# Kernel tuning notes

Measured on AMD Instinct MI355X. Metric: run time of the kernel, lower is better.

## Reference

```python
import jax, jax.numpy as jnp
import numpy as np

NUM_HEADS = 8
HEAD_SIZE = 64  # hidden_dim // num_heads = 512 // 8
SCALE = 1.0 / np.sqrt(HEAD_SIZE).astype(np.float32)
CAUSAL = True


def setup_inputs() -> dict:
    key = jax.random.key(0)
    k1, k2, k3 = jax.random.split(key, 3)
    b, s, d = 4, 2048, 512
    x = jax.random.normal(k1, (b, s, d), dtype=jnp.float32)
    w_qkv = jax.random.normal(k2, (d, 3 * d), dtype=jnp.float32) * 0.02
    b_qkv = jnp.zeros((3 * d,), dtype=jnp.float32)
    w_out = jax.random.normal(k3, (d, d), dtype=jnp.float32) * 0.02
    b_out = jnp.zeros((d,), dtype=jnp.float32)
    return {"x": x, "w_qkv": w_qkv, "b_qkv": b_qkv, "w_out": w_out, "b_out": b_out}


def reference(x, w_qkv, b_qkv, w_out, b_out):
    b, s, d = x.shape
    h, hd = NUM_HEADS, HEAD_SIZE
    qkv = x @ w_qkv + b_qkv                      # (b, s, 3d)
    q, k, v = jnp.split(qkv, 3, axis=-1)
    # (b, s, d) -> (b, h, s, hd)
    q = q.reshape(b, s, h, hd).transpose(0, 2, 1, 3)
    k = k.reshape(b, s, h, hd).transpose(0, 2, 1, 3)
    v = v.reshape(b, s, h, hd).transpose(0, 2, 1, 3)
    scores = jnp.einsum('bhqd,bhkd->bhqk', q, k) * SCALE  # (b, h, s, s)
    if CAUSAL:
        causal_mask = jnp.triu(jnp.ones((s, s), dtype=bool), k=1)
        scores = jnp.where(causal_mask, -jnp.inf, scores)
    attn = jax.nn.softmax(scores, axis=-1)
    out = jnp.einsum('bhqk,bhkd->bhqd', attn, v)          # (b, h, s, hd)
    out = out.transpose(0, 2, 1, 3).reshape(b, s, d)
    return out @ w_out + b_out
```

## Files before the change

kernel.cpp:

```cpp
#include <hip/hip_runtime.h>
#include <hip/hip_bf16.h>

#define BATCH 4
#define SEQ   2048
#define DM    512
#define NH    8
#define HD    64
#define PART  (BATCH*NH*SEQ*HD)
#define QSCALE 0.18033688f

typedef unsigned short u16;
typedef unsigned int   u32;
typedef __bf16 bf16x8 __attribute__((ext_vector_type(8)));
typedef float  f32x4  __attribute__((ext_vector_type(4)));
typedef float  f32x16 __attribute__((ext_vector_type(16)));
typedef unsigned int u32x2 __attribute__((ext_vector_type(2)));

__device__ __forceinline__ u16 f2bf(float f) {
    union { float f; u32 u; } v; v.f = f;
    u32 r = v.u + 0x7fffu + ((v.u >> 16) & 1u);
    return (u16)(r >> 16);
}

__device__ __forceinline__ void glds16(const u16* g, u16* lds) {
    __builtin_amdgcn_global_load_lds(
        (const __attribute__((address_space(1))) void*)g,
        (__attribute__((address_space(3))) void*)lds, 16, 0, 0);
}

__device__ __forceinline__ void pl32swap(u32 &a, u32 &b) {
    u32x2 r = __builtin_amdgcn_permlane32_swap(a, b, false, false);
    a = r[0]; b = r[1];
}

__global__ __launch_bounds__(256) void prep_k(
    const float* __restrict__ x, u16* __restrict__ xb,
    const float* __restrict__ w_qkv, u16* __restrict__ t_qkv,
    const float* __restrict__ w_out, u16* __restrict__ t_out)
{
    __shared__ u16 Ts[64][72];
    const int z = blockIdx.z, bx = blockIdx.x, t = threadIdx.x;

    if (z == 0) {
        const int n8 = PART / 8;
        for (int i = bx * 256 + t; i < n8; i += 512 * 256) {
            float4 a = *(const float4*)(x + (size_t)i * 8);
            float4 b = *(const float4*)(x + (size_t)i * 8 + 4);
            union { uint4 v; u16 s[8]; } o;
            o.s[0] = f2bf(a.x); o.s[1] = f2bf(a.y);
            o.s[2] = f2bf(a.z); o.s[3] = f2bf(a.w);
            o.s[4] = f2bf(b.x); o.s[5] = f2bf(b.y);
            o.s[6] = f2bf(b.z); o.s[7] = f2bf(b.w);
            *(uint4*)(xb + (size_t)i * 8) = o.v;
        }
        return;
    }
    const int N = (z == 1) ? 3 * DM : DM;
    const int ntiles = N / 64;
    if (bx >= ntiles * 8) return;
    const float* W = (z == 1) ? w_qkv : w_out;
    u16* Wt = (z == 1) ? t_qkv : t_out;
    const int n0 = (bx % ntiles) * 64, k0 = (bx / ntiles) * 64;

    #pragma unroll
    for (int l = 0; l < 4; ++l) {
        int idx = l * 1024 + t * 4;
        int r = idx >> 6, c = idx & 63;
        float4 v = *(const float4*)(W + (size_t)(k0 + r) * N + n0 + c);
        Ts[c + 0][r] = f2bf(v.x);
        Ts[c + 1][r] = f2bf(v.y);
        Ts[c + 2][r] = f2bf(v.z);
        Ts[c + 3][r] = f2bf(v.w);
    }
    __syncthreads();
    #pragma unroll
    for (int l = 0; l < 2; ++l) {
        int idx = l * 256 + t;
        int row = idx >> 3, ch = idx & 7;
        *(uint4*)(Wt + (size_t)(n0 + row) * DM + k0 + ch * 8) =
            *(const uint4*)(&Ts[row][ch * 8]);
    }
}

template<int MODE>
__global__ __launch_bounds__(256) void gemm_k(
    const u16* __restrict__ A, const u16* __restrict__ Bt,
    const float* __restrict__ bias, void* __restrict__ outv,
    int M, int N, int K)
{
    constexpr int BM = (MODE == 1) ? 64 : 128;
    constexpr int NI = (MODE == 1) ? 2 : 4;

    __shared__ __align__(16) u16 As[2][BM * 32];
    __shared__ __align__(16) u16 Bs[2][128 * 32];

    const int tid  = threadIdx.x;
    const int bm0  = blockIdx.x * BM;
    const int bn0  = blockIdx.y * 128;
    const int wave = tid >> 6, lane = tid & 63;
    const int l16  = lane & 15, quad = lane >> 4;
    const int wr   = (MODE == 1) ? 0 : (wave & 1) * 64;
    const int wc   = (MODE == 1) ? wave * 32 : (wave >> 1) * 64;

    const int srow = (lane >> 2);
    const int scol = (lane & 3) * 8;
    const int arow = (MODE == 1) ? (wave * 16) : (wave * 32);
    const u16* Ag = A + (size_t)(bm0 + arow + srow) * K + scol;
    const u16* Bg = Bt + (size_t)(bn0 + wave * 32 + srow) * K + scol;
    const int wofsA = arow * 32;
    const int wofsB = (wave * 32) * 32;

    f32x4 acc[4][NI];
    #pragma unroll
    for (int i = 0; i < 4; ++i)
        #pragma unroll
        for (int j = 0; j < NI; ++j)
            acc[i][j] = (f32x4){0.f, 0.f, 0.f, 0.f};

    glds16(Ag, &As[0][wofsA]);
    if (MODE == 0) glds16(Ag + (size_t)16 * K, &As[0][wofsA + 16 * 32]);
    glds16(Bg,                  &Bs[0][wofsB]);
    glds16(Bg + (size_t)16 * K, &Bs[0][wofsB + 16 * 32]);
    __syncthreads();

    const int NIT = K >> 5;
    for (int it = 0; it < NIT; ++it) {
        const int cur = it & 1;
        if (it + 1 < NIT) {
            const int nx = cur ^ 1;
            const int k0 = (it + 1) << 5;
            glds16(Ag + k0, &As[nx][wofsA]);
            if (MODE == 0) glds16(Ag + k0 + (size_t)16 * K, &As[nx][wofsA + 16 * 32]);
            glds16(Bg + k0,                  &Bs[nx][wofsB]);
            glds16(Bg + k0 + (size_t)16 * K, &Bs[nx][wofsB + 16 * 32]);
        }

        bf16x8 af[4], bfr[NI];
        #pragma unroll
        for (int mi = 0; mi < 4; ++mi)
            af[mi] = *(const bf16x8*)(&As[cur][(wr + mi * 16 + l16) * 32 + quad * 8]);
        #pragma unroll
        for (int ni = 0; ni < NI; ++ni)
            bfr[ni] = *(const bf16x8*)(&Bs[cur][(wc + ni * 16 + l16) * 32 + quad * 8]);
        #pragma unroll
        for (int mi = 0; mi < 4; ++mi)
            #pragma unroll
            for (int ni = 0; ni < NI; ++ni)
                acc[mi][ni] = __builtin_amdgcn_mfma_f32_16x16x32_bf16(
                    af[mi], bfr[ni], acc[mi][ni], 0, 0, 0);
        __syncthreads();
    }

    #pragma unroll
    for (int mi = 0; mi < 4; ++mi) {
        #pragma unroll
        for (int ni = 0; ni < NI; ++ni) {
            int col = bn0 + wc + ni * 16 + l16;
            float bv = bias[col];
            int row0 = bm0 + wr + mi * 16 + quad * 4;
            float v[4];
            #pragma unroll
            for (int reg = 0; reg < 4; ++reg) v[reg] = acc[mi][ni][reg] + bv;

            if (MODE == 1) {
                #pragma unroll
                for (int reg = 0; reg < 4; ++reg)
                    ((float*)outv)[(size_t)(row0 + reg) * N + col] = v[reg];
            } else {
                u16* ws = (u16*)outv;
                int part = col >> 9, wi = col & 511;
                int h = wi >> 6, e = wi & 63;
                int b = row0 >> 11, s0 = row0 & 2047;
                if (part == 2) {
                    union { u16 q[4]; uint2 u; } pk;
                    #pragma unroll
                    for (int reg = 0; reg < 4; ++reg) pk.q[reg] = f2bf(v[reg]);
                    *(uint2*)(ws + (size_t)2 * PART +
                              ((size_t)(b * NH + h) * HD + e) * SEQ + s0) = pk.u;
                } else {
                    float scl = (part == 0) ? QSCALE : 1.0f;
                    #pragma unroll
                    for (int reg = 0; reg < 4; ++reg)
                        ws[(size_t)part * PART +
                           ((size_t)(b * NH + h) * SEQ + s0 + reg) * HD + e] =
                            f2bf(v[reg] * scl);
                }
            }
        }
    }
}

__global__ __launch_bounds__(256, 4) void attn_k(
    const u16* __restrict__ Q, const u16* __restrict__ K,
    const u16* __restrict__ Vt, u16* __restrict__ O)
{
    __shared__ __align__(16) u16 KsB[2][64 * 64];
    __shared__ __align__(16) u16 VtB[2][64 * 64];
    __shared__ float Lred[4][32];

    const int bh = blockIdx.x;
    const int qt = 31 - blockIdx.y;
    const int tid = threadIdx.x, wave = tid >> 6, lane = tid & 63;
    const int l31 = lane & 31, hi = lane >> 5, x7 = lane & 7;
    const int qh = wave >> 1, kh = wave & 1;
    const size_t baseK = (size_t)bh * SEQ * HD;
    const size_t baseV = (size_t)bh * HD * SEQ;
    const int b = bh >> 3, h = bh & 7;

    const int sub = lane >> 3;
    const int lcx = (lane & 7) ^ sub;
    const u16* kg = K  + baseK + (size_t)((wave * 16 + sub) * 64)   + lcx * 8;
    const u16* vg = Vt + baseV + (size_t)((wave * 16 + sub) * 2048) + lcx * 8;
    u16* ksd = &KsB[0][wave * 1024];
    u16* vtd = &VtB[0][wave * 1024];

    int koff[4], voff[2][2];
    #pragma unroll
    for (int k = 0; k < 4; ++k)
        koff[k] = (kh * 32 + l31) * 64 + ((((k << 1) + hi)) ^ x7) * 8;
    #pragma unroll
    for (int dt = 0; dt < 2; ++dt)
        #pragma unroll
        for (int k0 = 0; k0 < 2; ++k0)
            voff[dt][k0] = (dt * 32 + l31) * 64 + ((kh * 4 + k0 * 2 + hi) ^ x7) * 8;

    const u16* qg = Q + baseK + (size_t)(qt * 64 + qh * 32 + l31) * 64 + hi * 8;
    bf16x8 qf[4];
    #pragma unroll
    for (int k = 0; k < 4; ++k)
        qf[k] = *(const bf16x8*)(qg + k * 16);

    glds16(kg,            ksd);
    glds16(kg + 8 * 64,   ksd + 512);
    glds16(vg,            vtd);
    glds16(vg + 8 * 2048, vtd + 512);
    __syncthreads();

    float la0 = 0.f, la1 = 0.f;
    f32x16 o0, o1;
    #pragma unroll
    for (int i = 0; i < 16; ++i) { o0[i] = 0.f; o1[i] = 0.f; }

    for (int kt = 0; kt <= qt; ++kt) {
        const int cur = kt & 1;
        if (kt < qt) {
            const int nx = (cur ^ 1) * 4096;
            glds16(kg + (size_t)(kt + 1) * 4096,          ksd + nx);
            glds16(kg + (size_t)(kt + 1) * 4096 + 8 * 64, ksd + nx + 512);
            glds16(vg + (size_t)(kt + 1) * 64,            vtd + nx);
            glds16(vg + (size_t)(kt + 1) * 64 + 8 * 2048, vtd + nx + 512);
        }

        const bool diag = (kt == qt);
        if (!(diag && kh > qh)) {
            bf16x8 kf[4], vf[2][2];
            #pragma unroll
            for (int k = 0; k < 4; ++k)
                kf[k] = *(const bf16x8*)(&KsB[cur][koff[k]]);
            #pragma unroll
            for (int dt = 0; dt < 2; ++dt)
                #pragma unroll
                for (int k0 = 0; k0 < 2; ++k0)
                    vf[dt][k0] = *(const bf16x8*)(&VtB[cur][voff[dt][k0]]);

            f32x16 st;
            #pragma unroll
            for (int i = 0; i < 16; ++i) st[i] = 0.f;
            __builtin_amdgcn_s_setprio(1);
            #pragma unroll
            for (int k = 0; k < 4; ++k)
                st = __builtin_amdgcn_mfma_f32_32x32x16_bf16(
                    kf[k], qf[k], st, 0, 0, 0);
            __builtin_amdgcn_s_setprio(0);

            float p[16];
            #pragma unroll
            for (int r = 0; r < 16; ++r)
                p[r] = __builtin_amdgcn_exp2f(st[r]);
            if (diag && kh == qh) {
                #pragma unroll
                for (int r = 0; r < 16; ++r) {
                    int kvl = (r & 3) + 8 * (r >> 2) + 4 * hi;
                    if (kvl > l31) p[r] = 0.f;
                }
            }
            #pragma unroll
            for (int r = 0; r < 8; ++r) { la0 += p[r]; la1 += p[r + 8]; }

            u32 c[8];
            #pragma unroll
            for (int m = 0; m < 8; ++m) {
                __hip_bfloat162 t =
                    __float22bfloat162_rn(float2{p[2 * m], p[2 * m + 1]});
                c[m] = *(u32*)&t;
            }
            pl32swap(c[0], c[2]); pl32swap(c[1], c[3]);
            pl32swap(c[4], c[6]); pl32swap(c[5], c[7]);
            union { u32 w[4]; bf16x8 v; } pa0, pa1;
            pa0.w[0] = c[0]; pa0.w[1] = c[1]; pa0.w[2] = c[2]; pa0.w[3] = c[3];
            pa1.w[0] = c[4]; pa1.w[1] = c[5]; pa1.w[2] = c[6]; pa1.w[3] = c[7];

            __builtin_amdgcn_s_setprio(1);
            o0 = __builtin_amdgcn_mfma_f32_32x32x16_bf16(pa0.v, vf[0][0], o0, 0, 0, 0);
            o0 = __builtin_amdgcn_mfma_f32_32x32x16_bf16(pa1.v, vf[0][1], o0, 0, 0, 0);
            o1 = __builtin_amdgcn_mfma_f32_32x32x16_bf16(pa0.v, vf[1][0], o1, 0, 0, 0);
            o1 = __builtin_amdgcn_mfma_f32_32x32x16_bf16(pa1.v, vf[1][1], o1, 0, 0, 0);
            __builtin_amdgcn_s_setprio(0);
        }
        __syncthreads();
    }

    float l2 = (la0 + la1);
    l2 += __shfl_xor(l2, 32);
    if (lane < 32) Lred[wave][lane] = l2;
    float* Ob = (qh == 0) ? (float*)&KsB[0][0] : (float*)&VtB[0][0];
    if (kh == 1) {
        #pragma unroll
        for (int r = 0; r < 16; ++r) {
            Ob[r * 64 + lane]        = o0[r];
            Ob[(16 + r) * 64 + lane] = o1[r];
        }
    }
    __syncthreads();
    if (kh == 0) {
        #pragma unroll
        for (int r = 0; r < 16; ++r) {
            int ql = (r & 3) + 8 * (r >> 2) + 4 * hi;
            float lt = Lred[2 * qh][ql] + Lred[2 * qh + 1][ql];
            int srow = qt * 64 + qh * 32 + ql;
            size_t idx = (((size_t)(b * SEQ + srow)) * NH + h) * HD + l31;
            float v0 = (o0[r] + Ob[r * 64 + lane]) / lt;
            float v1 = (o1[r] + Ob[(16 + r) * 64 + lane]) / lt;
            O[idx]      = f2bf(v0);
            O[idx + 32] = f2bf(v1);
        }
    }
}

extern "C" void kernel_launch(void* const* d_in, const int* in_sizes, int n_in,
                              void* d_out, int out_size, void* d_ws, size_t ws_size,
                              hipStream_t stream) {
    const float* x     = (const float*)d_in[0];
    const float* w_qkv = (const float*)d_in[1];
    const float* b_qkv = (const float*)d_in[2];
    const float* w_out = (const float*)d_in[3];
    const float* b_out = (const float*)d_in[4];

    u16* qkv    = (u16*)d_ws;
    u16* attn   = qkv + (size_t)3 * PART;
    u16* xb     = attn + (size_t)PART;
    u16* wt_qkv = xb + (size_t)PART;
    u16* wt_out = wt_qkv + (size_t)(3 * DM) * DM;

    const int M = BATCH * SEQ;

    prep_k<<<dim3(512, 1, 3), 256, 0, stream>>>(x, xb, w_qkv, wt_qkv,
                                                w_out, wt_out);

    dim3 g1(M / 128, (3 * DM) / 128);
    gemm_k<0><<<g1, 256, 0, stream>>>(xb, wt_qkv, b_qkv, qkv, M, 3 * DM, DM);

    dim3 g2(BATCH * NH, 32);
    attn_k<<<g2, 256, 0, stream>>>(qkv, qkv + PART, qkv + 2 * (size_t)PART, attn);

    dim3 g3(M / 64, DM / 128);
    gemm_k<1><<<g3, 256, 0, stream>>>(attn, wt_out, b_out, (float*)d_out, M, DM, DM);
}
```

Before: 145.8 us.

## Load K/V fragments directly from global memory, dropping LDS staging and barriers

The attention kernel no longer stages K and Vt tiles through double-buffered shared memory with async global-to-LDS copies. Each wave now reads its MFMA operands straight from global memory (relying on L1/L2) and skips the per-iteration __syncthreads. Waves that have no diagonal work stop one iteration earlier instead of idling through the barrier. This removes barrier and LDS traffic but gives up explicit prefetch overlap, and each K/V element is now read from global by two waves instead of once per block.

```diff
diff --git a/kernel.cpp b/kernel.cpp
--- a/kernel.cpp
+++ b/kernel.cpp
@@ -194,35 +194,20 @@
     const u16* __restrict__ Q, const u16* __restrict__ K,
     const u16* __restrict__ Vt, u16* __restrict__ O)
 {
-    __shared__ __align__(16) u16 KsB[2][64 * 64];
-    __shared__ __align__(16) u16 VtB[2][64 * 64];
+    __shared__ float Ob[2][2048];
     __shared__ float Lred[4][32];
 
     const int bh = blockIdx.x;
     const int qt = 31 - blockIdx.y;
     const int tid = threadIdx.x, wave = tid >> 6, lane = tid & 63;
-    const int l31 = lane & 31, hi = lane >> 5, x7 = lane & 7;
+    const int l31 = lane & 31, hi = lane >> 5;
     const int qh = wave >> 1, kh = wave & 1;
     const size_t baseK = (size_t)bh * SEQ * HD;
     const size_t baseV = (size_t)bh * HD * SEQ;
     const int b = bh >> 3, h = bh & 7;
 
-    const int sub = lane >> 3;
-    const int lcx = (lane & 7) ^ sub;
-    const u16* kg = K  + baseK + (size_t)((wave * 16 + sub) * 64)   + lcx * 8;
-    const u16* vg = Vt + baseV + (size_t)((wave * 16 + sub) * 2048) + lcx * 8;
-    u16* ksd = &KsB[0][wave * 1024];
-    u16* vtd = &VtB[0][wave * 1024];
-
-    int koff[4], voff[2][2];
-    #pragma unroll
-    for (int k = 0; k < 4; ++k)
-        koff[k] = (kh * 32 + l31) * 64 + ((((k << 1) + hi)) ^ x7) * 8;
-    #pragma unroll
-    for (int dt = 0; dt < 2; ++dt)
-        #pragma unroll
-        for (int k0 = 0; k0 < 2; ++k0)
-            voff[dt][k0] = (dt * 32 + l31) * 64 + ((kh * 4 + k0 * 2 + hi) ^ x7) * 8;
+    const u16* kgr = K  + baseK + (size_t)(kh * 32 + l31) * 64 + hi * 8;
+    const u16* vgr = Vt + baseV + (size_t)l31 * 2048 + (kh * 4 + hi) * 8;
 
     const u16* qg = Q + baseK + (size_t)(qt * 64 + qh * 32 + l31) * 64 + hi * 8;
     bf16x8 qf[4];
@@ -230,95 +215,78 @@
     for (int k = 0; k < 4; ++k)
         qf[k] = *(const bf16x8*)(qg + k * 16);
 
-    glds16(kg,            ksd);
-    glds16(kg + 8 * 64,   ksd + 512);
-    glds16(vg,            vtd);
-    glds16(vg + 8 * 2048, vtd + 512);
-    __syncthreads();
-
     float la0 = 0.f, la1 = 0.f;
     f32x16 o0, o1;
     #pragma unroll
     for (int i = 0; i < 16; ++i) { o0[i] = 0.f; o1[i] = 0.f; }
 
-    for (int kt = 0; kt <= qt; ++kt) {
-        const int cur = kt & 1;
-        if (kt < qt) {
-            const int nx = (cur ^ 1) * 4096;
-            glds16(kg + (size_t)(kt + 1) * 4096,          ksd + nx);
-            glds16(kg + (size_t)(kt + 1) * 4096 + 8 * 64, ksd + nx + 512);
-            glds16(vg + (size_t)(kt + 1) * 64,            vtd + nx);
-            glds16(vg + (size_t)(kt + 1) * 64 + 8 * 2048, vtd + nx + 512);
-        }
-
-        const bool diag = (kt == qt);
-        if (!(diag && kh > qh)) {
-            bf16x8 kf[4], vf[2][2];
+    const int kend = (kh > qh) ? qt : qt + 1;
+    for (int kt = 0; kt < kend; ++kt) {
+        const u16* kp = kgr + (size_t)kt * 4096;
+        const u16* vp = vgr + (size_t)kt * 64;
+        bf16x8 kf[4], vf[2][2];
+        #pragma unroll
+        for (int k = 0; k < 4; ++k)
+            kf[k] = *(const bf16x8*)(kp + k * 16);
+        #pragma unroll
+        for (int dt = 0; dt < 2; ++dt)
             #pragma unroll
-            for (int k = 0; k < 4; ++k)
-                kf[k] = *(const bf16x8*)(&KsB[cur][koff[k]]);
+            for (int k0 = 0; k0 < 2; ++k0)
+                vf[dt][k0] = *(const bf16x8*)(vp + dt * 65536 + k0 * 16);
+
+        f32x16 st;
+        #pragma unroll
+        for (int i = 0; i < 16; ++i) st[i] = 0.f;
+        __builtin_amdgcn_s_setprio(1);
+        #pragma unroll
+        for (int k = 0; k < 4; ++k)
+            st = __builtin_amdgcn_mfma_f32_32x32x16_bf16(
+                kf[k], qf[k], st, 0, 0, 0);
+        __builtin_amdgcn_s_setprio(0);
+
+        float p[16];
+        #pragma unroll
+        for (int r = 0; r < 16; ++r)
+            p[r] = __builtin_amdgcn_exp2f(st[r]);
+        if (kt == qt && kh == qh) {
             #pragma unroll
-            for (int dt = 0; dt < 2; ++dt)
-                #pragma unroll
-                for (int k0 = 0; k0 < 2; ++k0)
-                    vf[dt][k0] = *(const bf16x8*)(&VtB[cur][voff[dt][k0]]);
-
-            f32x16 st;
-            #pragma unroll
-            for (int i = 0; i < 16; ++i) st[i] = 0.f;
-            __builtin_amdgcn_s_setprio(1);
-            #pragma unroll
-            for (int k = 0; k < 4; ++k)
-                st = __builtin_amdgcn_mfma_f32_32x32x16_bf16(
-                    kf[k], qf[k], st, 0, 0, 0);
-            __builtin_amdgcn_s_setprio(0);
-
-            float p[16];
-            #pragma unroll
-            for (int r = 0; r < 16; ++r)
-                p[r] = __builtin_amdgcn_exp2f(st[r]);
-            if (diag && kh == qh) {
-                #pragma unroll
-                for (int r = 0; r < 16; ++r) {
-                    int kvl = (r & 3) + 8 * (r >> 2) + 4 * hi;
-                    if (kvl > l31) p[r] = 0.f;
-                }
+            for (int r = 0; r < 16; ++r) {
+                int kvl = (r & 3) + 8 * (r >> 2) + 4 * hi;
+                if (kvl > l31) p[r] = 0.f;
             }
-            #pragma unroll
-            for (int r = 0; r < 8; ++r) { la0 += p[r]; la1 += p[r + 8]; }
-
-            u32 c[8];
-            #pragma unroll
-            for (int m = 0; m < 8; ++m) {
-                __hip_bfloat162 t =
-                    __float22bfloat162_rn(float2{p[2 * m], p[2 * m + 1]});
-                c[m] = *(u32*)&t;
-            }
-            pl32swap(c[0], c[2]); pl32swap(c[1], c[3]);
-            pl32swap(c[4], c[6]); pl32swap(c[5], c[7]);
-            union { u32 w[4]; bf16x8 v; } pa0, pa1;
-            pa0.w[0] = c[0]; pa0.w[1] = c[1]; pa0.w[2] = c[2]; pa0.w[3] = c[3];
-            pa1.w[0] = c[4]; pa1.w[1] = c[5]; pa1.w[2] = c[6]; pa1.w[3] = c[7];
-
-            __builtin_amdgcn_s_setprio(1);
-            o0 = __builtin_amdgcn_mfma_f32_32x32x16_bf16(pa0.v, vf[0][0], o0, 0, 0, 0);
-            o0 = __builtin_amdgcn_mfma_f32_32x32x16_bf16(pa1.v, vf[0][1], o0, 0, 0, 0);
-            o1 = __builtin_amdgcn_mfma_f32_32x32x16_bf16(pa0.v, vf[1][0], o1, 0, 0, 0);
-            o1 = __builtin_amdgcn_mfma_f32_32x32x16_bf16(pa1.v, vf[1][1], o1, 0, 0, 0);
-            __builtin_amdgcn_s_setprio(0);
-        }
-        __syncthreads();
+        }
+        #pragma unroll
+        for (int r = 0; r < 8; ++r) { la0 += p[r]; la1 += p[r + 8]; }
+
+        u32 c[8];
+        #pragma unroll
+        for (int m = 0; m < 8; ++m) {
+            __hip_bfloat162 t =
+                __float22bfloat162_rn(float2{p[2 * m], p[2 * m + 1]});
+            c[m] = *(u32*)&t;
+        }
+        pl32swap(c[0], c[2]); pl32swap(c[1], c[3]);
+        pl32swap(c[4], c[6]); pl32swap(c[5], c[7]);
+        union { u32 w[4]; bf16x8 v; } pa0, pa1;
+        pa0.w[0] = c[0]; pa0.w[1] = c[1]; pa0.w[2] = c[2]; pa0.w[3] = c[3];
+        pa1.w[0] = c[4]; pa1.w[1] = c[5]; pa1.w[2] = c[6]; pa1.w[3] = c[7];
+
+        __builtin_amdgcn_s_setprio(1);
+        o0 = __builtin_amdgcn_mfma_f32_32x32x16_bf16(pa0.v, vf[0][0], o0, 0, 0, 0);
+        o0 = __builtin_amdgcn_mfma_f32_32x32x16_bf16(pa1.v, vf[0][1], o0, 0, 0, 0);
+        o1 = __builtin_amdgcn_mfma_f32_32x32x16_bf16(pa0.v, vf[1][0], o1, 0, 0, 0);
+        o1 = __builtin_amdgcn_mfma_f32_32x32x16_bf16(pa1.v, vf[1][1], o1, 0, 0, 0);
+        __builtin_amdgcn_s_setprio(0);
     }
 
     float l2 = (la0 + la1);
     l2 += __shfl_xor(l2, 32);
     if (lane < 32) Lred[wave][lane] = l2;
-    float* Ob = (qh == 0) ? (float*)&KsB[0][0] : (float*)&VtB[0][0];
     if (kh == 1) {
         #pragma unroll
         for (int r = 0; r < 16; ++r) {
-            Ob[r * 64 + lane]        = o0[r];
-            Ob[(16 + r) * 64 + lane] = o1[r];
+            Ob[qh][r * 64 + lane]        = o0[r];
+            Ob[qh][(16 + r) * 64 + lane] = o1[r];
         }
     }
     __syncthreads();
@@ -329,8 +297,8 @@
             float lt = Lred[2 * qh][ql] + Lred[2 * qh + 1][ql];
             int srow = qt * 64 + qh * 32 + ql;
             size_t idx = (((size_t)(b * SEQ + srow)) * NH + h) * HD + l31;
-            float v0 = (o0[r] + Ob[r * 64 + lane]) / lt;
-            float v1 = (o1[r] + Ob[(16 + r) * 64 + lane]) / lt;
+            float v0 = (o0[r] + Ob[qh][r * 64 + lane]) / lt;
+            float v1 = (o1[r] + Ob[qh][(16 + r) * 64 + lane]) / lt;
             O[idx]      = f2bf(v0);
             O[idx + 32] = f2bf(v1);
         }
```

Measured after the change: 186.1 us. +27.6%, slower.

## Widen attention blocks to 128 query rows with eight waves sharing K/V tiles

Applied to the files above, without the earlier changes.

The attention kernel now runs 512 threads per block, covering 128 query rows (four query sub-tiles times two key halves) instead of 64, and launches half as many blocks. Each K/V tile staged into LDS is reused by twice as many query rows, which halves global K/V loads per query, and each wave issues one async copy per tile instead of two. The trade-offs are coarser causal work balance, since waves whose query sub-tile is earlier sit idle on late key tiles, fewer blocks to fill the GPU, and higher per-block resource use under launch bounds of 512 threads.

```diff
diff --git a/kernel.cpp b/kernel.cpp
--- a/kernel.cpp
+++ b/kernel.cpp
@@ -190,16 +190,16 @@
     }
 }
 
-__global__ __launch_bounds__(256, 4) void attn_k(
+__global__ __launch_bounds__(512, 4) void attn_k(
     const u16* __restrict__ Q, const u16* __restrict__ K,
     const u16* __restrict__ Vt, u16* __restrict__ O)
 {
     __shared__ __align__(16) u16 KsB[2][64 * 64];
     __shared__ __align__(16) u16 VtB[2][64 * 64];
-    __shared__ float Lred[4][32];
+    __shared__ float Lred[8][32];
 
     const int bh = blockIdx.x;
-    const int qt = 31 - blockIdx.y;
+    const int qb = 15 - blockIdx.y;
     const int tid = threadIdx.x, wave = tid >> 6, lane = tid & 63;
     const int l31 = lane & 31, hi = lane >> 5, x7 = lane & 7;
     const int qh = wave >> 1, kh = wave & 1;
@@ -207,12 +207,12 @@
     const size_t baseV = (size_t)bh * HD * SEQ;
     const int b = bh >> 3, h = bh & 7;
 
-    const int sub = lane >> 3;
-    const int lcx = (lane & 7) ^ sub;
-    const u16* kg = K  + baseK + (size_t)((wave * 16 + sub) * 64)   + lcx * 8;
-    const u16* vg = Vt + baseV + (size_t)((wave * 16 + sub) * 2048) + lcx * 8;
-    u16* ksd = &KsB[0][wave * 1024];
-    u16* vtd = &VtB[0][wave * 1024];
+    const int sub8 = lane >> 3;
+    const int lcx  = (lane & 7) ^ sub8;
+    const u16* kg = K  + baseK + (size_t)((wave * 8 + sub8) * 64)   + lcx * 8;
+    const u16* vg = Vt + baseV + (size_t)((wave * 8 + sub8) * 2048) + lcx * 8;
+    u16* ksd = &KsB[0][wave * 512];
+    u16* vtd = &VtB[0][wave * 512];
 
     int koff[4], voff[2][2];
     #pragma unroll
@@ -224,16 +224,14 @@
         for (int k0 = 0; k0 < 2; ++k0)
             voff[dt][k0] = (dt * 32 + l31) * 64 + ((kh * 4 + k0 * 2 + hi) ^ x7) * 8;
 
-    const u16* qg = Q + baseK + (size_t)(qt * 64 + qh * 32 + l31) * 64 + hi * 8;
+    const u16* qg = Q + baseK + (size_t)(qb * 128 + qh * 32 + l31) * 64 + hi * 8;
     bf16x8 qf[4];
     #pragma unroll
     for (int k = 0; k < 4; ++k)
         qf[k] = *(const bf16x8*)(qg + k * 16);
 
-    glds16(kg,            ksd);
-    glds16(kg + 8 * 64,   ksd + 512);
-    glds16(vg,            vtd);
-    glds16(vg + 8 * 2048, vtd + 512);
+    glds16(kg, ksd);
+    glds16(vg, vtd);
     __syncthreads();
 
     float la0 = 0.f, la1 = 0.f;
@@ -241,18 +239,18 @@
     #pragma unroll
     for (int i = 0; i < 16; ++i) { o0[i] = 0.f; o1[i] = 0.f; }
 
-    for (int kt = 0; kt <= qt; ++kt) {
+    const int lim = 4 * qb + qh;
+    const int NT  = 2 * qb + 2;
+    for (int kt = 0; kt < NT; ++kt) {
         const int cur = kt & 1;
-        if (kt < qt) {
+        if (kt + 1 < NT) {
             const int nx = (cur ^ 1) * 4096;
-            glds16(kg + (size_t)(kt + 1) * 4096,          ksd + nx);
-            glds16(kg + (size_t)(kt + 1) * 4096 + 8 * 64, ksd + nx + 512);
-            glds16(vg + (size_t)(kt + 1) * 64,            vtd + nx);
-            glds16(vg + (size_t)(kt + 1) * 64 + 8 * 2048, vtd + nx + 512);
-        }
-
-        const bool diag = (kt == qt);
-        if (!(diag && kh > qh)) {
+            glds16(kg + (size_t)(kt + 1) * 4096, ksd + nx);
+            glds16(vg + (size_t)(kt + 1) * 64,   vtd + nx);
+        }
+
+        const int tk = 2 * kt + kh;
+        if (tk <= lim) {
             bf16x8 kf[4], vf[2][2];
             #pragma unroll
             for (int k = 0; k < 4; ++k)
@@ -277,7 +275,7 @@
             #pragma unroll
             for (int r = 0; r < 16; ++r)
                 p[r] = __builtin_amdgcn_exp2f(st[r]);
-            if (diag && kh == qh) {
+            if (tk == lim) {
                 #pragma unroll
                 for (int r = 0; r < 16; ++r) {
                     int kvl = (r & 3) + 8 * (r >> 2) + 4 * hi;
@@ -313,7 +311,8 @@
     float l2 = (la0 + la1);
     l2 += __shfl_xor(l2, 32);
     if (lane < 32) Lred[wave][lane] = l2;
-    float* Ob = (qh == 0) ? (float*)&KsB[0][0] : (float*)&VtB[0][0];
+    float* Ob = ((qh & 2) ? (float*)&VtB[0][0] : (float*)&KsB[0][0])
+                + (qh & 1) * 2048;
     if (kh == 1) {
         #pragma unroll
         for (int r = 0; r < 16; ++r) {
@@ -327,7 +326,7 @@
         for (int r = 0; r < 16; ++r) {
             int ql = (r & 3) + 8 * (r >> 2) + 4 * hi;
             float lt = Lred[2 * qh][ql] + Lred[2 * qh + 1][ql];
-            int srow = qt * 64 + qh * 32 + ql;
+            int srow = qb * 128 + qh * 32 + ql;
             size_t idx = (((size_t)(b * SEQ + srow)) * NH + h) * HD + l31;
             float v0 = (o0[r] + Ob[r * 64 + lane]) / lt;
             float v1 = (o1[r] + Ob[(16 + r) * 64 + lane]) / lt;
@@ -360,8 +359,8 @@
     dim3 g1(M / 128, (3 * DM) / 128);
     gemm_k<0><<<g1, 256, 0, stream>>>(xb, wt_qkv, b_qkv, qkv, M, 3 * DM, DM);
 
-    dim3 g2(BATCH * NH, 32);
-    attn_k<<<g2, 256, 0, stream>>>(qkv, qkv + PART, qkv + 2 * (size_t)PART, attn);
+    dim3 g2(BATCH * NH, 16);
+    attn_k<<<g2, 512, 0, stream>>>(qkv, qkv + PART, qkv + 2 * (size_t)PART, attn);
 
     dim3 g3(M / 64, DM / 128);
     gemm_k<1><<<g3, 256, 0, stream>>>(attn, wt_out, b_out, (float*)d_out, M, DM, DM);
```

Result: slower. 151.3 us (+3.7%).

## Use 128-row query tiles with each wave owning full KV tile

Applied to the files above, without the earlier changes.

The attention kernel now processes 128 query rows per block instead of 64, and each of the four waves owns a 32-row query slice across the full 64-key tile. This replaces the previous split of key halves across waves, so the cross-wave LDS reduction of partial outputs and row sums goes away. Each K/V tile loaded into LDS is reused by twice as many query rows, which halves K/V global traffic. The cost is half as many blocks, more registers per wave (two score tiles, eight V fragments), and more idle waves on the diagonal tiles where masked waves skip work.

```diff
diff --git a/kernel.cpp b/kernel.cpp
--- a/kernel.cpp
+++ b/kernel.cpp
@@ -199,10 +199,10 @@
     __shared__ float Lred[4][32];
 
     const int bh = blockIdx.x;
-    const int qt = 31 - blockIdx.y;
+    const int qb = 15 - blockIdx.y;
     const int tid = threadIdx.x, wave = tid >> 6, lane = tid & 63;
     const int l31 = lane & 31, hi = lane >> 5, x7 = lane & 7;
-    const int qh = wave >> 1, kh = wave & 1;
+    const int qh = wave;
     const size_t baseK = (size_t)bh * SEQ * HD;
     const size_t baseV = (size_t)bh * HD * SEQ;
     const int b = bh >> 3, h = bh & 7;
@@ -214,17 +214,19 @@
     u16* ksd = &KsB[0][wave * 1024];
     u16* vtd = &VtB[0][wave * 1024];
 
-    int koff[4], voff[2][2];
-    #pragma unroll
-    for (int k = 0; k < 4; ++k)
-        koff[k] = (kh * 32 + l31) * 64 + ((((k << 1) + hi)) ^ x7) * 8;
+    int koff[2][4], voff[2][4];
+    #pragma unroll
+    for (int kvh = 0; kvh < 2; ++kvh)
+        #pragma unroll
+        for (int k = 0; k < 4; ++k)
+            koff[kvh][k] = (kvh * 32 + l31) * 64 + (((k << 1) + hi) ^ x7) * 8;
     #pragma unroll
     for (int dt = 0; dt < 2; ++dt)
         #pragma unroll
-        for (int k0 = 0; k0 < 2; ++k0)
-            voff[dt][k0] = (dt * 32 + l31) * 64 + ((kh * 4 + k0 * 2 + hi) ^ x7) * 8;
-
-    const u16* qg = Q + baseK + (size_t)(qt * 64 + qh * 32 + l31) * 64 + hi * 8;
+        for (int s = 0; s < 4; ++s)
+            voff[dt][s] = (dt * 32 + l31) * 64 + (((s << 1) + hi) ^ x7) * 8;
+
+    const u16* qg = Q + baseK + (size_t)(qb * 128 + qh * 32 + l31) * 64 + hi * 8;
     bf16x8 qf[4];
     #pragma unroll
     for (int k = 0; k < 4; ++k)
@@ -241,9 +243,11 @@
     #pragma unroll
     for (int i = 0; i < 16; ++i) { o0[i] = 0.f; o1[i] = 0.f; }
 
-    for (int kt = 0; kt <= qt; ++kt) {
+    const int mylim = 2 * qb + (qh >> 1);
+    const int NT = 2 * qb + 2;
+    for (int kt = 0; kt < NT; ++kt) {
         const int cur = kt & 1;
-        if (kt < qt) {
+        if (kt + 1 < NT) {
             const int nx = (cur ^ 1) * 4096;
             glds16(kg + (size_t)(kt + 1) * 4096,          ksd + nx);
             glds16(kg + (size_t)(kt + 1) * 4096 + 8 * 64, ksd + nx + 512);
@@ -251,60 +255,90 @@
             glds16(vg + (size_t)(kt + 1) * 64 + 8 * 2048, vtd + nx + 512);
         }
 
-        const bool diag = (kt == qt);
-        if (!(diag && kh > qh)) {
-            bf16x8 kf[4], vf[2][2];
+        if (kt <= mylim) {
+            bf16x8 kf[4];
+            f32x16 st0, st1;
+            #pragma unroll
+            for (int i = 0; i < 16; ++i) { st0[i] = 0.f; st1[i] = 0.f; }
             #pragma unroll
             for (int k = 0; k < 4; ++k)
-                kf[k] = *(const bf16x8*)(&KsB[cur][koff[k]]);
-            #pragma unroll
-            for (int dt = 0; dt < 2; ++dt)
-                #pragma unroll
-                for (int k0 = 0; k0 < 2; ++k0)
-                    vf[dt][k0] = *(const bf16x8*)(&VtB[cur][voff[dt][k0]]);
-
-            f32x16 st;
-            #pragma unroll
-            for (int i = 0; i < 16; ++i) st[i] = 0.f;
+                kf[k] = *(const bf16x8*)(&KsB[cur][koff[0][k]]);
             __builtin_amdgcn_s_setprio(1);
             #pragma unroll
             for (int k = 0; k < 4; ++k)
-                st = __builtin_amdgcn_mfma_f32_32x32x16_bf16(
-                    kf[k], qf[k], st, 0, 0, 0);
+                st0 = __builtin_amdgcn_mfma_f32_32x32x16_bf16(
+                    kf[k], qf[k], st0, 0, 0, 0);
             __builtin_amdgcn_s_setprio(0);
-
-            float p[16];
-            #pragma unroll
-            for (int r = 0; r < 16; ++r)
-                p[r] = __builtin_amdgcn_exp2f(st[r]);
-            if (diag && kh == qh) {
-                #pragma unroll
-                for (int r = 0; r < 16; ++r) {
-                    int kvl = (r & 3) + 8 * (r >> 2) + 4 * hi;
-                    if (kvl > l31) p[r] = 0.f;
+            #pragma unroll
+            for (int k = 0; k < 4; ++k)
+                kf[k] = *(const bf16x8*)(&KsB[cur][koff[1][k]]);
+            __builtin_amdgcn_s_setprio(1);
+            #pragma unroll
+            for (int k = 0; k < 4; ++k)
+                st1 = __builtin_amdgcn_mfma_f32_32x32x16_bf16(
+                    kf[k], qf[k], st1, 0, 0, 0);
+            __builtin_amdgcn_s_setprio(0);
+
+            float p[32];
+            #pragma unroll
+            for (int r = 0; r < 16; ++r) {
+                p[r]      = __builtin_amdgcn_exp2f(st0[r]);
+                p[16 + r] = __builtin_amdgcn_exp2f(st1[r]);
+            }
+            if (kt == mylim) {
+                if ((qh & 1) == 0) {
+                    #pragma unroll
+                    for (int r = 0; r < 16; ++r) {
+                        int kvl = (r & 3) + 8 * (r >> 2) + 4 * hi;
+                        if (kvl > l31) p[r] = 0.f;
+                        p[16 + r] = 0.f;
+                    }
+                } else {
+                    #pragma unroll
+                    for (int r = 0; r < 16; ++r) {
+                        int kvl = (r & 3) + 8 * (r >> 2) + 4 * hi;
+                        if (kvl > l31) p[16 + r] = 0.f;
+                    }
                 }
             }
             #pragma unroll
-            for (int r = 0; r < 8; ++r) { la0 += p[r]; la1 += p[r + 8]; }
-
-            u32 c[8];
+            for (int r = 0; r < 16; ++r) { la0 += p[r]; la1 += p[16 + r]; }
+
+            u32 c[8], d[8];
             #pragma unroll
             for (int m = 0; m < 8; ++m) {
-                __hip_bfloat162 t =
+                __hip_bfloat162 t0 =
                     __float22bfloat162_rn(float2{p[2 * m], p[2 * m + 1]});
-                c[m] = *(u32*)&t;
+                __hip_bfloat162 t1 =
+                    __float22bfloat162_rn(float2{p[16 + 2 * m], p[16 + 2 * m + 1]});
+                c[m] = *(u32*)&t0;
+                d[m] = *(u32*)&t1;
             }
             pl32swap(c[0], c[2]); pl32swap(c[1], c[3]);
             pl32swap(c[4], c[6]); pl32swap(c[5], c[7]);
-            union { u32 w[4]; bf16x8 v; } pa0, pa1;
+            pl32swap(d[0], d[2]); pl32swap(d[1], d[3]);
+            pl32swap(d[4], d[6]); pl32swap(d[5], d[7]);
+            union { u32 w[4]; bf16x8 v; } pa0, pa1, pa2, pa3;
             pa0.w[0] = c[0]; pa0.w[1] = c[1]; pa0.w[2] = c[2]; pa0.w[3] = c[3];
             pa1.w[0] = c[4]; pa1.w[1] = c[5]; pa1.w[2] = c[6]; pa1.w[3] = c[7];
-
+            pa2.w[0] = d[0]; pa2.w[1] = d[1]; pa2.w[2] = d[2]; pa2.w[3] = d[3];
+            pa3.w[0] = d[4]; pa3.w[1] = d[5]; pa3.w[2] = d[6]; pa3.w[3] = d[7];
+
+            bf16x8 vf0[4], vf1[4];
+            #pragma unroll
+            for (int s = 0; s < 4; ++s) {
+                vf0[s] = *(const bf16x8*)(&VtB[cur][voff[0][s]]);
+                vf1[s] = *(const bf16x8*)(&VtB[cur][voff[1][s]]);
+            }
             __builtin_amdgcn_s_setprio(1);
-            o0 = __builtin_amdgcn_mfma_f32_32x32x16_bf16(pa0.v, vf[0][0], o0, 0, 0, 0);
-            o0 = __builtin_amdgcn_mfma_f32_32x32x16_bf16(pa1.v, vf[0][1], o0, 0, 0, 0);
-            o1 = __builtin_amdgcn_mfma_f32_32x32x16_bf16(pa0.v, vf[1][0], o1, 0, 0, 0);
-            o1 = __builtin_amdgcn_mfma_f32_32x32x16_bf16(pa1.v, vf[1][1], o1, 0, 0, 0);
+            o0 = __builtin_amdgcn_mfma_f32_32x32x16_bf16(pa0.v, vf0[0], o0, 0, 0, 0);
+            o0 = __builtin_amdgcn_mfma_f32_32x32x16_bf16(pa1.v, vf0[1], o0, 0, 0, 0);
+            o0 = __builtin_amdgcn_mfma_f32_32x32x16_bf16(pa2.v, vf0[2], o0, 0, 0, 0);
+            o0 = __builtin_amdgcn_mfma_f32_32x32x16_bf16(pa3.v, vf0[3], o0, 0, 0, 0);
+            o1 = __builtin_amdgcn_mfma_f32_32x32x16_bf16(pa0.v, vf1[0], o1, 0, 0, 0);
+            o1 = __builtin_amdgcn_mfma_f32_32x32x16_bf16(pa1.v, vf1[1], o1, 0, 0, 0);
+            o1 = __builtin_amdgcn_mfma_f32_32x32x16_bf16(pa2.v, vf1[2], o1, 0, 0, 0);
+            o1 = __builtin_amdgcn_mfma_f32_32x32x16_bf16(pa3.v, vf1[3], o1, 0, 0, 0);
             __builtin_amdgcn_s_setprio(0);
         }
         __syncthreads();
@@ -313,27 +347,14 @@
     float l2 = (la0 + la1);
     l2 += __shfl_xor(l2, 32);
     if (lane < 32) Lred[wave][lane] = l2;
-    float* Ob = (qh == 0) ? (float*)&KsB[0][0] : (float*)&VtB[0][0];
-    if (kh == 1) {
-        #pragma unroll
-        for (int r = 0; r < 16; ++r) {
-            Ob[r * 64 + lane]        = o0[r];
-            Ob[(16 + r) * 64 + lane] = o1[r];
-        }
-    }
-    __syncthreads();
-    if (kh == 0) {
-        #pragma unroll
-        for (int r = 0; r < 16; ++r) {
-            int ql = (r & 3) + 8 * (r >> 2) + 4 * hi;
-            float lt = Lred[2 * qh][ql] + Lred[2 * qh + 1][ql];
-            int srow = qt * 64 + qh * 32 + ql;
-            size_t idx = (((size_t)(b * SEQ + srow)) * NH + h) * HD + l31;
-            float v0 = (o0[r] + Ob[r * 64 + lane]) / lt;
-            float v1 = (o1[r] + Ob[(16 + r) * 64 + lane]) / lt;
-            O[idx]      = f2bf(v0);
-            O[idx + 32] = f2bf(v1);
-        }
+    #pragma unroll
+    for (int r = 0; r < 16; ++r) {
+        int ql = (r & 3) + 8 * (r >> 2) + 4 * hi;
+        float lt = Lred[wave][ql];
+        int srow = qb * 128 + qh * 32 + ql;
+        size_t idx = (((size_t)(b * SEQ + srow)) * NH + h) * HD + l31;
+        O[idx]      = f2bf(o0[r] / lt);
+        O[idx + 32] = f2bf(o1[r] / lt);
     }
 }
 
@@ -360,7 +381,7 @@
     dim3 g1(M / 128, (3 * DM) / 128);
     gemm_k<0><<<g1, 256, 0, stream>>>(xb, wt_qkv, b_qkv, qkv, M, 3 * DM, DM);
 
-    dim3 g2(BATCH * NH, 32);
+    dim3 g2(BATCH * NH, 16);
     attn_k<<<g2, 256, 0, stream>>>(qkv, qkv + PART, qkv + 2 * (size_t)PART, attn);
 
     dim3 g3(M / 64, DM / 128);
```

After: 175.0 us. +20.0%, slower.
